# Kernel optimization log

Measured on AMD Instinct MI355X. Metric: run time of the kernel, lower is better.

The kernel has to match this reference:

```python
import jax, jax.numpy as jnp
import numpy as np

B, L, N, DM = 32, 12, 883, 64
DSP, DTP, H, HID, HOR = 128, 128, 4, 64, 12
E_SPA = 14128
ENC_LAYERS = 3
HIDDEN = 5 * HID  # 2*embed + node + tid + diw = 320


def _gat(x, es, et, W, a_s, a_d, bias, edge_att=None):
    # GATConv-style attention with optional per-edge info-bottleneck mask (gat_ib)
    n = x.shape[0]
    h = (x @ W).reshape(n, H, -1)            # [n,H,Dh]
    sc_s = (h * a_s).sum(-1)                 # [n,H]
    sc_d = (h * a_d).sum(-1)
    al = jax.nn.leaky_relu(sc_s[es] + sc_d[et], 0.2)   # [E,H]
    al = al - jax.ops.segment_max(al, et, num_segments=n)[et]
    ex = jnp.exp(al)
    a = ex / jax.ops.segment_sum(ex, et, num_segments=n)[et]
    if edge_att is not None:
        a = a * edge_att[:, None]
    out = jax.ops.segment_sum(a[..., None] * h[es], et, num_segments=n)
    return out.reshape(n, -1) + bias


def _gsat(x, ei, gat_p, ext_p):
    # GSAT: embed -> extractor MLP on edge endpoint pairs -> sigmoid edge att -> masked conv
    es, et = ei[0], ei[1]
    emb = _gat(x, es, et, *gat_p)
    w1, b1, w2, b2, w3, b3 = ext_p
    f = jnp.concatenate([emb[es], emb[et]], axis=-1)
    logit = (jax.nn.relu(jax.nn.relu(f @ w1 + b1) @ w2 + b2) @ w3 + b3)[:, 0]
    att = jax.nn.sigmoid(logit)  # eval-mode (no concrete-relaxation sampling)
    return _gat(x, es, et, *gat_p, edge_att=att)


def setup_inputs():
    key = jax.random.key(0)
    ks = iter(jax.random.split(key, 80))
    def nrm(shape, s=0.02):
        return jax.random.normal(next(ks), shape, jnp.float32) * s
    hist = jax.random.normal(next(ks), (B, L, N, 3), jnp.float32)
    tid = jax.random.randint(next(ks), (B, L, N), 0, 288).astype(jnp.float32)
    diw = jax.random.randint(next(ks), (B, L, N), 0, 7).astype(jnp.float32)
    hist = hist.at[..., 1].set(tid).at[..., 2].set(diw)
    ei_spa = jax.random.randint(next(ks), (2, E_SPA), 0, N).astype(jnp.int32)
    g = jnp.arange(L, dtype=jnp.int32)
    ei_temp = jnp.stack([jnp.repeat(g, L), jnp.tile(g, L)])  # dense lag x lag temporal graph
    inp = dict(history_data=hist, edge_idx_spa=ei_spa, edge_idx_temp=ei_temp)
    inp.update(
        node_emb=nrm((N, HID)), tid_emb=nrm((288, HID)), diw_emb=nrm((7, HID)),
        start_w=nrm((3, DM)), start_b=jnp.zeros((DM,), jnp.float32),
        ts_w=nrm((DM * L, HID)), ts_b=jnp.zeros((HID,), jnp.float32),
        tr_spat_w=nrm((L * DM, DSP)), tr_spat_b=jnp.zeros((DSP,), jnp.float32),
        inv_spat_w=nrm((DSP, L * DM)), inv_spat_b=jnp.zeros((L * DM,), jnp.float32),
        tr_temp_w=nrm((N * DM, DTP)), tr_temp_b=jnp.zeros((DTP,), jnp.float32),
        inv_temp_w=nrm((DTP, N * DM)), inv_temp_b=jnp.zeros((N * DM,), jnp.float32),
        gat_sp_w=nrm((DSP, DSP)), gat_sp_asrc=nrm((H, DSP // H)), gat_sp_adst=nrm((H, DSP // H)), gat_sp_bias=jnp.zeros((DSP,), jnp.float32),
        ext_sp_w1=nrm((2 * DSP, 4 * DSP)), ext_sp_b1=jnp.zeros((4 * DSP,), jnp.float32),
        ext_sp_w2=nrm((4 * DSP, DSP)), ext_sp_b2=jnp.zeros((DSP,), jnp.float32),
        ext_sp_w3=nrm((DSP, 1)), ext_sp_b3=jnp.zeros((1,), jnp.float32),
        gat_tp_w=nrm((DTP, DTP)), gat_tp_asrc=nrm((H, DTP // H)), gat_tp_adst=nrm((H, DTP // H)), gat_tp_bias=jnp.zeros((DTP,), jnp.float32),
        ext_tp_w1=nrm((2 * DTP, 4 * DTP)), ext_tp_b1=jnp.zeros((4 * DTP,), jnp.float32),
        ext_tp_w2=nrm((4 * DTP, DTP)), ext_tp_b2=jnp.zeros((DTP,), jnp.float32),
        ext_tp_w3=nrm((DTP, 1)), ext_tp_b3=jnp.zeros((1,), jnp.float32),
        enc_w1=nrm((ENC_LAYERS, HIDDEN, HIDDEN)), enc_b1=jnp.zeros((ENC_LAYERS, HIDDEN), jnp.float32),
        enc_w2=nrm((ENC_LAYERS, HIDDEN, HIDDEN)), enc_b2=jnp.zeros((ENC_LAYERS, HIDDEN), jnp.float32),
        reg_w=nrm((HIDDEN, HOR)), reg_b=jnp.zeros((HOR,), jnp.float32),
    )
    return inp


def reference(history_data, edge_idx_spa, edge_idx_temp, node_emb, tid_emb, diw_emb,
              start_w, start_b, ts_w, ts_b,
              tr_spat_w, tr_spat_b, inv_spat_w, inv_spat_b,
              tr_temp_w, tr_temp_b, inv_temp_w, inv_temp_b,
              gat_sp_w, gat_sp_asrc, gat_sp_adst, gat_sp_bias,
              ext_sp_w1, ext_sp_b1, ext_sp_w2, ext_sp_b2, ext_sp_w3, ext_sp_b3,
              gat_tp_w, gat_tp_asrc, gat_tp_adst, gat_tp_bias,
              ext_tp_w1, ext_tp_b1, ext_tp_w2, ext_tp_b2, ext_tp_w3, ext_tp_b3,
              enc_w1, enc_b1, enc_w2, enc_b2, reg_w, reg_b):
    b, l, n = history_data.shape[:3]
    tid = jax.lax.stop_gradient(history_data[:, -1, :, 1]).astype(jnp.int32)
    diw = jax.lax.stop_gradient(history_data[:, -1, :, 2]).astype(jnp.int32)
    X = history_data[..., :3] @ start_w + start_b           # [B,L,N,DM]
    res = X.transpose(0, 2, 1, 3).reshape(b, n, l * DM)      # [B,N,L*DM]
    ts_res = res @ ts_w + ts_b                               # conv1x1 over nodes == per-node linear
    gp_sp = (gat_sp_w, gat_sp_asrc, gat_sp_adst, gat_sp_bias)
    ep_sp = (ext_sp_w1, ext_sp_b1, ext_sp_w2, ext_sp_b2, ext_sp_w3, ext_sp_b3)
    gp_tp = (gat_tp_w, gat_tp_asrc, gat_tp_adst, gat_tp_bias)
    ep_tp = (ext_tp_w1, ext_tp_b1, ext_tp_w2, ext_tp_b2, ext_tp_w3, ext_tp_b3)
    # batch_st_gsat: per-sample spatial GSAT then temporal GSAT (vmapped instead of Python loop)
    spa_in = res @ tr_spat_w + tr_spat_b                     # [B,N,DSP]
    spa_out = jax.vmap(lambda xx: _gsat(xx, edge_idx_spa, gp_sp, ep_sp))(spa_in)
    spa_back = (spa_out @ inv_spat_w + inv_spat_b).reshape(b, n, l, DM).transpose(0, 2, 1, 3)
    temp_in = spa_back.reshape(b, l, n * DM) @ tr_temp_w + tr_temp_b   # [B,L,DTP]
    temp_out = jax.vmap(lambda xx: _gsat(xx, edge_idx_temp, gp_tp, ep_tp))(temp_in)
    temp_back = (temp_out @ inv_temp_w + inv_temp_b).reshape(b, l, n, DM)
    ts_temp = temp_back.transpose(0, 2, 1, 3).reshape(b, n, l * DM) @ ts_w + ts_b
    hid = jnp.concatenate([
        ts_res, ts_temp,
        jnp.broadcast_to(node_emb, (b, n, HID)),
        tid_emb[tid], diw_emb[diw],
    ], axis=-1)                                              # [B,N,320]
    for i in range(ENC_LAYERS):  # MLP_res: x + fc2(relu(fc1(x)))
        hid = hid + jax.nn.relu(hid @ enc_w1[i] + enc_b1[i]) @ enc_w2[i] + enc_b2[i]
    pred = hid @ reg_w + reg_b                               # [B,N,HOR]
    return pred.transpose(0, 2, 1)[..., None]                # [B,HOR,N,1]
```

## Files before the change

kernel.cpp:

```cpp
#include <hip/hip_runtime.h>
#include <hip/hip_bf16.h>
#include <cstdint>
#include <cstddef>

#define B_   32
#define L_   12
#define N_   883
#define DM_  64
#define E_SP 14128
#define E_TP 144
#define NT_  12
#define RBN  28256
#define RBL  384
#define LDM  768
#define NDM  56512

static inline int cdiv_h(int a, int b){ return (a+b-1)/b; }

__device__ __forceinline__ ushort f2bf(float f){
    unsigned u = __float_as_uint(f);
    unsigned lsb = (u >> 16) & 1u;
    u += 0x7fffu + lsb;
    return (ushort)(u >> 16);
}
__device__ __forceinline__ float bf2f(ushort h){
    return __uint_as_float(((unsigned)h) << 16);
}
__device__ __forceinline__ ushort f2h(float f){
    _Float16 h = (_Float16)f;
    ushort r; __builtin_memcpy(&r, &h, 2);
    return r;
}

typedef __bf16 bf16x8 __attribute__((ext_vector_type(8)));
typedef _Float16 f16x8 __attribute__((ext_vector_type(8)));
typedef _Float16 f16x2 __attribute__((ext_vector_type(2)));
typedef float  f32x4  __attribute__((ext_vector_type(4)));
typedef short  s16x2  __attribute__((ext_vector_type(2)));
union BF8 { bf16x8 v; ushort u[8]; unsigned w[4]; int4 i; };
union HF8 { f16x8 v; ushort u[8]; unsigned w[4]; int4 i; };

__device__ __forceinline__ unsigned pkrelu(unsigned x){
    s16x2 v;
    __builtin_memcpy(&v, &x, 4);
    s16x2 z = 0;
    v = __builtin_elementwise_max(v, z);
    unsigned r;
    __builtin_memcpy(&r, &v, 4);
    return r;
}
__device__ __forceinline__ unsigned pkaddh(unsigned x, unsigned y){
    f16x2 a, b;
    __builtin_memcpy(&a, &x, 4);
    __builtin_memcpy(&b, &y, 4);
    a = a + b;
    unsigned r;
    __builtin_memcpy(&r, &a, 4);
    return r;
}

__global__ void k_res(const float* __restrict__ hist, const float* __restrict__ sw,
                      const float* __restrict__ sb, ushort* __restrict__ resHi,
                      ushort* __restrict__ resLo)
{
    int idx = blockIdx.x*256 + threadIdx.x;
    if (idx >= RBN*LDM) return;
    int r = idx / LDM, col = idx - r*LDM;
    int b = r / N_, n = r - b*N_;
    int l = col >> 6, d = col & 63;
    const float* hp = hist + ((size_t)(b*L_ + l)*N_ + n)*3;
    float v = hp[0]*sw[d] + hp[1]*sw[64+d] + hp[2]*sw[128+d] + sb[d];
    ushort hi = f2bf(v);
    resHi[idx] = hi;
    resLo[idx] = f2bf(v - bf2f(hi));
}

template<int CT, int AMODE, int EPI, bool RELU, bool RES>
__launch_bounds__(256)
__global__ void mgemm(const ushort* __restrict__ A, const ushort* __restrict__ WT,
                      const float* __restrict__ bias, float* __restrict__ resF,
                      void* __restrict__ outP, int M, int N, int K)
{
    const int t = threadIdx.x, wv = t >> 6, l = t & 63;
    const int lr = l & 15, lk = l >> 4;
    const int row0 = blockIdx.y*64 + wv*16;
    const int col0 = blockIdx.x * (CT*16);
    int arr = row0 + lr; if (arr >= M) arr = M-1;
    int ab = 0, an = 0;
    if (AMODE == 1) { ab = arr / N_; an = arr - ab*N_; }
    const ushort* ap = A + (size_t)arr*K + lk*8;
    f32x4 acc[CT] = {};
    for (int k0 = 0; k0 < K; k0 += 32) {
        BF8 af;
        if (AMODE == 0) af.i = *(const int4*)(ap + k0);
        else {
            int k = k0 + lk*8; int ll = k >> 6, d = k & 63;
            af.i = *(const int4*)(A + ((size_t)(ab*L_ + ll))*NDM + (size_t)an*64 + d);
        }
        #pragma unroll
        for (int ct = 0; ct < CT; ++ct) {
            BF8 bf; bf.i = *(const int4*)&WT[(size_t)(col0 + ct*16 + lr)*K + k0 + lk*8];
            acc[ct] = __builtin_amdgcn_mfma_f32_16x16x32_bf16(af.v, bf.v, acc[ct], 0, 0, 0);
        }
    }
    #pragma unroll
    for (int ct = 0; ct < CT; ++ct) {
        int c = col0 + ct*16 + lr;
        float bv = 0.f;
        if (EPI == 2) { if (bias && c < 12) bv = bias[c]; }
        else if (bias) bv = bias[c];
        #pragma unroll
        for (int g = 0; g < 4; ++g) {
            int r = row0 + lk*4 + g;
            if (r >= M) continue;
            float v = acc[ct][g] + bv;
            if (RELU) v = fmaxf(v, 0.f);
            if (RES) {
                v += resF[(size_t)r*N + c];
                resF[(size_t)r*N + c] = v;
            }
            if (EPI == 0) {
                ((ushort*)outP)[(size_t)r*N + c] = f2bf(v);
            } else if (EPI == 1) {
                ((float*)outP)[(size_t)r*N + c] = v;
            } else if (EPI == 2) {
                if (c < 12) {
                    int b = r / N_, n = r - (r/N_)*N_;
                    ((float*)outP)[((size_t)(b*L_ + c))*N_ + n] = v;
                }
            } else {
                int b = r / N_, n = r - (r/N_)*N_;
                ((ushort*)outP)[((size_t)(b*L_ + (c>>6)))*NDM + (size_t)n*64 + (c&63)] = f2bf(v);
            }
        }
    }
}

template<int RT, int CT, int EPI, bool RELU, bool RES>
__launch_bounds__(256)
__global__ void mgemm_rt(const ushort* __restrict__ A, const ushort* __restrict__ WT,
                         const float* __restrict__ bias, float* __restrict__ resF,
                         void* __restrict__ outP, int M, int N, int K)
{
    const int t = threadIdx.x, wv = t >> 6, l = t & 63;
    const int lr = l & 15, lk = l >> 4;
    const int rowbase = blockIdx.y*(4*RT*16) + wv*(RT*16);
    const int col0 = blockIdx.x * (CT*16);
    const ushort* ap[RT];
    #pragma unroll
    for (int rt = 0; rt < RT; ++rt) {
        int arr = rowbase + rt*16 + lr; if (arr >= M) arr = M-1;
        ap[rt] = A + (size_t)arr*K + lk*8;
    }
    f32x4 acc[RT][CT] = {};
    for (int k0 = 0; k0 < K; k0 += 32) {
        BF8 af[RT];
        #pragma unroll
        for (int rt = 0; rt < RT; ++rt) af[rt].i = *(const int4*)(ap[rt] + k0);
        #pragma unroll
        for (int ct = 0; ct < CT; ++ct) {
            BF8 bf; bf.i = *(const int4*)&WT[(size_t)(col0 + ct*16 + lr)*K + k0 + lk*8];
            #pragma unroll
            for (int rt = 0; rt < RT; ++rt)
                acc[rt][ct] = __builtin_amdgcn_mfma_f32_16x16x32_bf16(af[rt].v, bf.v,
                                                                     acc[rt][ct], 0, 0, 0);
        }
    }
    #pragma unroll
    for (int rt = 0; rt < RT; ++rt)
        #pragma unroll
        for (int ct = 0; ct < CT; ++ct) {
            int c = col0 + ct*16 + lr;
            float bv = bias ? bias[c] : 0.f;
            #pragma unroll
            for (int g = 0; g < 4; ++g) {
                int r = rowbase + rt*16 + lk*4 + g;
                if (r >= M) continue;
                float v = acc[rt][ct][g] + bv;
                if (RELU) v = fmaxf(v, 0.f);
                if (RES) {
                    v += resF[(size_t)r*N + c];
                    resF[(size_t)r*N + c] = v;
                }
                if (EPI == 0) {
                    ((ushort*)outP)[(size_t)r*N + c] = f2bf(v);
                } else if (EPI == 1) {
                    ((float*)outP)[(size_t)r*N + c] = v;
                } else if (EPI == 4) {
                    ((ushort*)outP)[(size_t)r*N + c] = f2h(v);
                } else {
                    int b = r / N_, n = r - (r/N_)*N_;
                    ((ushort*)outP)[((size_t)(b*L_ + (c>>6)))*NDM + (size_t)n*64 + (c&63)] = f2bf(v);
                }
            }
        }
}

template<int CT>
__launch_bounds__(256)
__global__ void mgemm_hl(const ushort* __restrict__ Ahi, const ushort* __restrict__ Alo,
                         const ushort* __restrict__ WThi, const ushort* __restrict__ WTlo,
                         const float* __restrict__ bias, float* __restrict__ outF,
                         int M, int N, int K)
{
    const int t = threadIdx.x, wv = t >> 6, l = t & 63;
    const int lr = l & 15, lk = l >> 4;
    const int row0 = blockIdx.y*64 + wv*16;
    const int col0 = blockIdx.x * (CT*16);
    int arr = row0 + lr; if (arr >= M) arr = M-1;
    const ushort* aph = Ahi + (size_t)arr*K + lk*8;
    const ushort* apl = Alo + (size_t)arr*K + lk*8;
    f32x4 acc[CT] = {};
    for (int k0 = 0; k0 < K; k0 += 32) {
        BF8 ah, al_;
        ah.i  = *(const int4*)(aph + k0);
        al_.i = *(const int4*)(apl + k0);
        #pragma unroll
        for (int ct = 0; ct < CT; ++ct) {
            size_t wo = (size_t)(col0 + ct*16 + lr)*K + k0 + lk*8;
            BF8 bh, bl;
            bh.i = *(const int4*)&WThi[wo];
            bl.i = *(const int4*)&WTlo[wo];
            acc[ct] = __builtin_amdgcn_mfma_f32_16x16x32_bf16(ah.v,  bh.v, acc[ct], 0, 0, 0);
            acc[ct] = __builtin_amdgcn_mfma_f32_16x16x32_bf16(al_.v, bh.v, acc[ct], 0, 0, 0);
            acc[ct] = __builtin_amdgcn_mfma_f32_16x16x32_bf16(ah.v,  bl.v, acc[ct], 0, 0, 0);
        }
    }
    #pragma unroll
    for (int ct = 0; ct < CT; ++ct) {
        int c = col0 + ct*16 + lr;
        float bv = bias ? bias[c] : 0.f;
        #pragma unroll
        for (int g = 0; g < 4; ++g) {
            int r = row0 + lk*4 + g;
            if (r >= M) continue;
            outF[(size_t)r*N + c] = acc[ct][g] + bv;
        }
    }
}

#define TCH 1024
__launch_bounds__(256)
__global__ void temp_in_mfma(const ushort* __restrict__ AT, const ushort* __restrict__ WtT,
                             float* __restrict__ out)
{
    const int t = threadIdx.x, wv = t >> 6, l = t & 63;
    const int lr = l & 15, lk = l >> 4;
    const int row0 = blockIdx.y * 96;
    const int c0 = wv * 32;
    const int k0b = blockIdx.x * TCH;
    const int kend = (k0b + TCH < NDM) ? (k0b + TCH) : NDM;
    f32x4 acc[6][2] = {};
    for (int k0 = k0b; k0 < kend; k0 += 32) {
        BF8 b0, b1;
        b0.i = *(const int4*)&WtT[(size_t)(c0 + lr)*NDM + k0 + lk*8];
        b1.i = *(const int4*)&WtT[(size_t)(c0 + 16 + lr)*NDM + k0 + lk*8];
        #pragma unroll
        for (int m = 0; m < 6; ++m) {
            BF8 af; af.i = *(const int4*)&AT[(size_t)(row0 + m*16 + lr)*NDM + k0 + lk*8];
            acc[m][0] = __builtin_amdgcn_mfma_f32_16x16x32_bf16(af.v, b0.v, acc[m][0], 0, 0, 0);
            acc[m][1] = __builtin_amdgcn_mfma_f32_16x16x32_bf16(af.v, b1.v, acc[m][1], 0, 0, 0);
        }
    }
    #pragma unroll
    for (int m = 0; m < 6; ++m)
        #pragma unroll
        for (int ct = 0; ct < 2; ++ct) {
            int c = c0 + ct*16 + lr;
            #pragma unroll
            for (int g = 0; g < 4; ++g) {
                int r = row0 + m*16 + lk*4 + g;
                atomicAdd(&out[(size_t)r*128 + c], acc[m][ct][g]);
            }
        }
}

__global__ void k_sc(const ushort* __restrict__ h, const float* __restrict__ as_,
                     const float* __restrict__ ad_, float* __restrict__ scs,
                     float* __restrict__ scd, int R)
{
    int r = blockIdx.x*256 + threadIdx.x;
    if (r >= R) return;
    const ushort* hr = h + (size_t)r*128;
    #pragma unroll
    for (int hh = 0; hh < 4; ++hh) {
        float ss = 0.f, sd = 0.f;
        #pragma unroll
        for (int k = 0; k < 32; ++k) {
            float hv = bf2f(hr[hh*32 + k]);
            ss += hv*as_[hh*32+k];
            sd += hv*ad_[hh*32+k];
        }
        scs[(size_t)r*4+hh] = ss;
        scd[(size_t)r*4+hh] = sd;
    }
}

__global__ void k_attE(const float* __restrict__ scs, const float* __restrict__ scd,
                       const int* __restrict__ ei, int E, int NN,
                       float* __restrict__ a_buf, float* __restrict__ nsum)
{
    int idx = blockIdx.x*256 + threadIdx.x;
    if (idx >= B_*E) return;
    int b = idx / E, e = idx - b*E;
    int s = ei[e], tg = ei[E+e];
    const float* ps = scs + (size_t)(b*NN+s)*4;
    const float* pd = scd + (size_t)(b*NN+tg)*4;
    float* ns = nsum + (size_t)(b*NN+tg)*4;
    float* pa = a_buf + (size_t)idx*4;
    #pragma unroll
    for (int hh = 0; hh < 4; ++hh) {
        float al = ps[hh] + pd[hh];
        al = al > 0.f ? al : 0.2f*al;
        float ex = expf(al);
        pa[hh] = ex;
        atomicAdd(ns + hh, ex);
    }
}

__global__ void k_count(const int* __restrict__ ei, int E, int* __restrict__ counts){
    int e = blockIdx.x*256 + threadIdx.x;
    if (e < E) atomicAdd(&counts[ei[E + e]], 1);
}
__global__ void k_scan(const int* __restrict__ counts, int* __restrict__ off,
                       int* __restrict__ cur, int n)
{
    __shared__ int s[1024];
    int t = threadIdx.x;
    int v0 = (t < n) ? counts[t] : 0;
    s[t] = v0;
    __syncthreads();
    for (int o = 1; o < 1024; o <<= 1) {
        int v = (t >= o) ? s[t-o] : 0;
        __syncthreads();
        s[t] += v;
        __syncthreads();
    }
    if (t < n) {
        off[t+1] = s[t];
        cur[t] = s[t] - v0;
        if (t == 0) off[0] = 0;
    }
}
__global__ void k_fill(const int* __restrict__ ei, int E, int* __restrict__ cur,
                       int* __restrict__ lst){
    int e = blockIdx.x*256 + threadIdx.x;
    if (e < E) {
        int pos = atomicAdd(&cur[ei[E+e]], 1);
        lst[pos] = e;
    }
}

template<bool USE_ATT>
__global__ void k_gather(const ushort* __restrict__ h, const float* __restrict__ a_buf,
                         const float* __restrict__ nsum, const float* __restrict__ att,
                         const int* __restrict__ ei, const int* __restrict__ off,
                         const int* __restrict__ lst, const float* __restrict__ bias,
                         ushort* __restrict__ out, int E, int NN)
{
    int bn = blockIdx.x*4 + (threadIdx.x >> 6);
    int b = bn / NN, n = bn - b*NN;
    int lane = threadIdx.x & 63;
    int c0 = lane*2;
    int hh = lane >> 4;
    float rn = 1.f / nsum[(size_t)bn*4 + hh];
    int o0 = off[n], o1 = off[n+1];
    float ax = 0.f, ay = 0.f;
    for (int i = o0; i < o1; ++i) {
        int e = lst[i];
        float a = a_buf[((size_t)b*E + e)*4 + hh] * rn;
        if (USE_ATT) a *= att[(size_t)b*E + e];
        int s = ei[e];
        unsigned hv = *(const unsigned*)&h[((size_t)b*NN + s)*128 + c0];
        ax += a * __uint_as_float(hv << 16);
        ay += a * __uint_as_float(hv & 0xffff0000u);
    }
    ushort2 o2;
    o2.x = f2bf(ax + bias[c0]);
    o2.y = f2bf(ay + bias[c0+1]);
    *(ushort2*)&out[(size_t)bn*128 + c0] = o2;
}

__global__ void k_prepW2(const float* __restrict__ W2, ushort* __restrict__ W2T)
{
    int idx = blockIdx.x*256 + threadIdx.x;
    if (idx >= 512*128) return;
    int k = idx >> 7, c = idx & 127;
    W2T[(size_t)c*512 + k] = f2h(W2[idx]);
}
__global__ void k_prepT(const float* __restrict__ W, ushort* __restrict__ WT, int K, int N)
{
    int idx = blockIdx.x*256 + threadIdx.x;
    if (idx >= K*N) return;
    int k = idx / N, c = idx - k*N;
    WT[(size_t)c*K + k] = f2bf(W[idx]);
}
__global__ void k_prepT_hl(const float* __restrict__ W, ushort* __restrict__ WThi,
                           ushort* __restrict__ WTlo, int K, int N)
{
    int idx = blockIdx.x*256 + threadIdx.x;
    if (idx >= K*N) return;
    int k = idx / N, c = idx - k*N;
    float v = W[idx];
    ushort hi = f2bf(v);
    WThi[(size_t)c*K + k] = hi;
    WTlo[(size_t)c*K + k] = f2bf(v - bf2f(hi));
}
__global__ void k_prepWtT(const float* __restrict__ W, ushort* __restrict__ WT)
{
    __shared__ ushort tile[128][129];
    int k0 = blockIdx.x * 128;
    int t = threadIdx.x;
    for (int i = t; i < 128*128; i += 256) {
        int k = i >> 7, c = i & 127;
        int kk = k0 + k;
        tile[c][k] = (kk < NDM) ? f2bf(W[(size_t)kk*128 + c]) : (ushort)0;
    }
    __syncthreads();
    for (int i = t; i < 128*128; i += 256) {
        int c = i >> 7, k = i & 127;
        int kk = k0 + k;
        if (kk < NDM) WT[(size_t)c*NDM + kk] = tile[c][k];
    }
}
__global__ void k_prepT_big(const float* __restrict__ W, ushort* __restrict__ WT)
{
    __shared__ float tile[128][65];
    int c0 = blockIdx.x * 64;
    int t = threadIdx.x;
    for (int i = t; i < 128*64; i += 256) {
        int k = i >> 6, ci = i & 63;
        tile[k][ci] = W[(size_t)k*NDM + c0 + ci];
    }
    __syncthreads();
    for (int i = t; i < 64*128; i += 256) {
        int ci = i >> 7, k = i & 127;
        WT[(size_t)(c0 + ci)*128 + k] = f2bf(tile[k][ci]);
    }
}
__global__ void k_bcat(const float* __restrict__ b1, float* __restrict__ dst){
    int i = blockIdx.x*256 + threadIdx.x;
    if (i < 1024) dst[i] = (i < 512) ? b1[i] : 0.f;
}

template<bool SWZ>
__launch_bounds__(256, 3)
__global__ void ext2_mfma(const ushort* __restrict__ PQ, const ushort* __restrict__ W2T,
                          const float* __restrict__ b2, const float* __restrict__ w3,
                          const float* __restrict__ b3p, const int* __restrict__ ei,
                          const int* __restrict__ lst,
                          float* __restrict__ att, int E, int NN, int nblk)
{
    __shared__ ushort Bs[2][128*40];
    int bid = blockIdx.x;
    if (SWZ) {
        bid = (blockIdx.x & 7) * (gridDim.x >> 3) + (blockIdx.x >> 3);
        if (bid >= nblk) bid = nblk - 1;
    }
    const int t = threadIdx.x;
    const int wv = t >> 6, l = t & 63;
    const int lr = l & 15, lk = l >> 4;

    const ushort* pr[2]; const ushort* qr[2];
    int row0[2];
    #pragma unroll
    for (int rt = 0; rt < 2; ++rt) {
        row0[rt] = bid*128 + wv*32 + rt*16;
        int r = row0[rt] + lr;
        int b = (int)((unsigned)r / (unsigned)E), i = r - b*E;
        int e = lst[i];
        pr[rt] = PQ + ((size_t)b*NN + ei[e])*1024 + lk*8;
        qr[rt] = PQ + ((size_t)b*NN + ei[E+e])*1024 + 512 + lk*8;
    }
    const int sc = t >> 1, sh = (t & 1) * 16;
    const ushort* wsrc = W2T + (size_t)sc*512 + sh;
    ushort* wd0 = &Bs[0][sc*40 + sh];
    ushort* wd1 = &Bs[1][sc*40 + sh];

    {
        int4 a0 = *(const int4*)(wsrc);
        int4 a1 = *(const int4*)(wsrc + 8);
        *(int4*)wd0 = a0;
        *(int4*)(wd0 + 8) = a1;
    }
    HF8 pu[2], qu[2];
    #pragma unroll
    for (int rt = 0; rt < 2; ++rt) {
        pu[rt].i = *(const int4*)(pr[rt]);
        qu[rt].i = *(const int4*)(qr[rt]);
    }
    int4 bnA = *(const int4*)(wsrc + 32);
    int4 bnB = *(const int4*)(wsrc + 40);
    __syncthreads();

    f32x4 acc[2][8] = {};
    for (int kc = 0; kc < 16; ++kc) {
        const int cb = kc & 1;
        HF8 af[2];
        #pragma unroll
        for (int rt = 0; rt < 2; ++rt)
            #pragma unroll
            for (int j = 0; j < 4; ++j)
                af[rt].w[j] = pkrelu(pkaddh(pu[rt].w[j], qu[rt].w[j]));
        {
            int ka = (kc+1 < 15) ? kc+1 : 15;
            #pragma unroll
            for (int rt = 0; rt < 2; ++rt) {
                pu[rt].i = *(const int4*)(pr[rt] + ka*32);
                qu[rt].i = *(const int4*)(qr[rt] + ka*32);
            }
        }
        __builtin_amdgcn_s_setprio(1);
        #pragma unroll
        for (int ct = 0; ct < 8; ++ct) {
            HF8 bfm;
            bfm.v = *(const f16x8*)&Bs[cb][(ct*16 + lr)*40 + lk*8];
            #pragma unroll
            for (int rt = 0; rt < 2; ++rt)
                acc[rt][ct] = __builtin_amdgcn_mfma_f32_16x16x32_f16(af[rt].v, bfm.v,
                                                                    acc[rt][ct], 0, 0, 0);
        }
        __builtin_amdgcn_s_setprio(0);
        if (kc < 15) {
            ushort* wd = cb ? wd0 : wd1;
            *(int4*)wd = bnA;
            *(int4*)(wd + 8) = bnB;
        }
        {
            int kb = (kc+2 < 15) ? kc+2 : 15;
            bnA = *(const int4*)(wsrc + kb*32);
            bnB = *(const int4*)(wsrc + kb*32 + 8);
        }
        __syncthreads();
    }
    float b3 = b3p[0];
    #pragma unroll
    for (int rt = 0; rt < 2; ++rt) {
        float part[4] = {0.f,0.f,0.f,0.f};
        #pragma unroll
        for (int ct = 0; ct < 8; ++ct) {
            int c = ct*16 + lr;
            float b2v = b2[c], w3v = w3[c];
            #pragma unroll
            for (int g = 0; g < 4; ++g)
                part[g] += fmaxf(acc[rt][ct][g] + b2v, 0.f) * w3v;
        }
        #pragma unroll
        for (int m = 1; m < 16; m <<= 1)
            #pragma unroll
            for (int g = 0; g < 4; ++g)
                part[g] += __shfl_xor(part[g], m, 64);
        if (lr == 0) {
            #pragma unroll
            for (int g = 0; g < 4; ++g) {
                int rr = row0[rt] + lk*4 + g;
                int b = (int)((unsigned)rr / (unsigned)E), i = rr - b*E;
                int e = lst[i];
                att[(size_t)b*E + e] = 1.f/(1.f + expf(-(part[g] + b3)));
            }
        }
    }
}

__global__ void k_bias_fill(float* __restrict__ dst, const float* __restrict__ bias, int n){
    int i = blockIdx.x*256 + threadIdx.x;
    if (i < n) dst[i] = bias[i & 127];
}
__global__ void k_f2b(const float* __restrict__ src, ushort* __restrict__ dst, int n){
    int i = blockIdx.x*256 + threadIdx.x;
    if (i < n) dst[i] = f2bf(src[i]);
}

__global__ void k_hid(const float* __restrict__ ts_res, const float* __restrict__ ts_temp,
                      const float* __restrict__ node_emb, const float* __restrict__ tid_emb,
                      const float* __restrict__ diw_emb, const float* __restrict__ hist,
                      float* __restrict__ hid, ushort* __restrict__ hidB)
{
    int idx = blockIdx.x*256 + threadIdx.x;
    if (idx >= RBN*320) return;
    int r = idx / 320, c = idx - r*320;
    int b = r / N_, n = r - b*N_;
    float v;
    if (c < 64)        v = ts_res[(size_t)r*64 + c];
    else if (c < 128)  v = ts_temp[(size_t)r*64 + (c-64)];
    else if (c < 192)  v = node_emb[(size_t)n*64 + (c-128)];
    else if (c < 256) {
        int tid = (int)hist[((size_t)(b*L_ + (L_-1))*N_ + n)*3 + 1];
        v = tid_emb[(size_t)tid*64 + (c-192)];
    } else {
        int diw = (int)hist[((size_t)(b*L_ + (L_-1))*N_ + n)*3 + 2];
        v = diw_emb[(size_t)diw*64 + (c-256)];
    }
    hid[idx] = v;
    hidB[idx] = f2bf(v);
}

extern "C" void kernel_launch(void* const* d_in, const int* in_sizes, int n_in,
                              void* d_out, int out_size, void* d_ws, size_t ws_size,
                              hipStream_t stream)
{
    (void)in_sizes; (void)n_in; (void)out_size; (void)ws_size;
    const float* hist      = (const float*)d_in[0];
    const int*   ei_sp     = (const int*)  d_in[1];
    const int*   ei_tp     = (const int*)  d_in[2];
    const float* node_emb  = (const float*)d_in[3];
    const float* tid_emb   = (const float*)d_in[4];
    const float* diw_emb   = (const float*)d_in[5];
    const float* start_w   = (const float*)d_in[6];
    const float* start_b   = (const float*)d_in[7];
    const float* ts_w      = (const float*)d_in[8];
    const float* ts_b      = (const float*)d_in[9];
    const float* tr_spat_w = (const float*)d_in[10];
    const float* tr_spat_b = (const float*)d_in[11];
    const float* inv_spat_w= (const float*)d_in[12];
    const float* inv_spat_b= (const float*)d_in[13];
    const float* tr_temp_w = (const float*)d_in[14];
    const float* tr_temp_b = (const float*)d_in[15];
    const float* inv_temp_w= (const float*)d_in[16];
    const float* inv_temp_b= (const float*)d_in[17];
    const float* gat_sp_w  = (const float*)d_in[18];
    const float* gat_sp_as = (const float*)d_in[19];
    const float* gat_sp_ad = (const float*)d_in[20];
    const float* gat_sp_b  = (const float*)d_in[21];
    const float* ext_sp_w1 = (const float*)d_in[22];
    const float* ext_sp_b1 = (const float*)d_in[23];
    const float* ext_sp_w2 = (const float*)d_in[24];
    const float* ext_sp_b2 = (const float*)d_in[25];
    const float* ext_sp_w3 = (const float*)d_in[26];
    const float* ext_sp_b3 = (const float*)d_in[27];
    const float* gat_tp_w  = (const float*)d_in[28];
    const float* gat_tp_as = (const float*)d_in[29];
    const float* gat_tp_ad = (const float*)d_in[30];
    const float* gat_tp_b  = (const float*)d_in[31];
    const float* ext_tp_w1 = (const float*)d_in[32];
    const float* ext_tp_b1 = (const float*)d_in[33];
    const float* ext_tp_w2 = (const float*)d_in[34];
    const float* ext_tp_b2 = (const float*)d_in[35];
    const float* ext_tp_w3 = (const float*)d_in[36];
    const float* ext_tp_b3 = (const float*)d_in[37];
    const float* enc_w1    = (const float*)d_in[38];
    const float* enc_b1    = (const float*)d_in[39];
    const float* enc_w2    = (const float*)d_in[40];
    const float* enc_b2    = (const float*)d_in[41];
    const float* reg_w     = (const float*)d_in[42];
    const float* reg_b     = (const float*)d_in[43];
    float* out = (float*)d_out;

    size_t o = 0;
    char* wsb = (char*)d_ws;
    auto allocB = [&](size_t bytes) -> void* {
        void* p = wsb + o;
        o += (bytes + 255) & ~(size_t)255;
        return p;
    };
    void* bufA = allocB((size_t)RBN*768*2);
    void* bufB = allocB((size_t)RBN*768*2);
    void* bufC = allocB((size_t)RBN*512*2);
    void* bufD = allocB((size_t)RBN*320*2);
    float*  ts_res  = (float*)allocB((size_t)RBN*64*4);
    ushort* spaB    = (ushort*)allocB((size_t)RBN*128*2);
    ushort* hB      = (ushort*)allocB((size_t)RBN*128*2);
    float*  sc_s    = (float*)allocB((size_t)RBN*4*4);
    float*  sc_d    = (float*)allocB((size_t)RBN*4*4);
    float*  nsum    = (float*)allocB((size_t)RBN*4*4);
    float*  a_buf   = (float*)allocB((size_t)B_*E_SP*4*4);
    float*  att     = (float*)allocB((size_t)B_*E_SP*4);
    ushort* embB    = (ushort*)allocB((size_t)RBN*128*2);
    int*    csr     = (int*)allocB(17024*4);
    float*  temp_in = (float*)allocB((size_t)RBL*128*4);
    ushort* tempB   = (ushort*)allocB((size_t)RBL*128*2);
    ushort* toutB   = (ushort*)allocB((size_t)RBL*128*2);
    ushort* PQ_t    = (ushort*)allocB((size_t)RBL*1024*2);
    float*  ts_temp = (float*)allocB((size_t)RBN*64*4);
    ushort* W2T_sp  = (ushort*)allocB(512*128*2);
    ushort* W2T_tp  = (ushort*)allocB(512*128*2);
    ushort* WtT     = (ushort*)allocB((size_t)128*NDM*2);
    ushort* itWT    = (ushort*)allocB((size_t)NDM*128*2);
    ushort* tspWT   = (ushort*)allocB(128*768*2);
    ushort* ispWT   = (ushort*)allocB(768*128*2);
    ushort* gspWT   = (ushort*)allocB(128*128*2);
    ushort* gtpWT   = (ushort*)allocB(128*128*2);
    ushort* w1catT_sp = (ushort*)allocB((size_t)1024*128*2);
    ushort* w1catT_tp = (ushort*)allocB((size_t)1024*128*2);
    float*  b1cat_sp  = (float*)allocB(1024*4);
    float*  b1cat_tp  = (float*)allocB(1024*4);
    ushort* w1T_enc = (ushort*)allocB((size_t)3*320*320*2);
    ushort* w2T_enc = (ushort*)allocB((size_t)3*320*320*2);
    ushort* tswT_hi = (ushort*)allocB(64*768*2);
    ushort* tswT_lo = (ushort*)allocB(64*768*2);
    ushort* reg_wT  = (ushort*)allocB(16*320*2);

    ushort* resHi = (ushort*)bufA;
    ushort* resLo = (ushort*)bufB;
    ushort* AT    = (ushort*)bufA;
    float*  hid   = (float*)bufA;
    ushort* PQ_sp = (ushort*)bufB;
    ushort* tback = (ushort*)bufB;
    ushort* hidB  = (ushort*)bufC;
    ushort* R1b   = (ushort*)bufD;

    int* counts_sp = csr;
    int* off_sp    = csr + 883;
    int* cur_sp    = csr + 1767;
    int* list_sp   = csr + 2650;
    int* counts_tp = csr + 16778;
    int* off_tp    = csr + 16790;
    int* cur_tp    = csr + 16803;
    int* list_tp   = csr + 16815;

    hipMemsetAsync(counts_sp, 0, 883*4, stream);
    k_count<<<cdiv_h(E_SP,256),256,0,stream>>>(ei_sp, E_SP, counts_sp);
    k_scan<<<1,1024,0,stream>>>(counts_sp, off_sp, cur_sp, 883);
    k_fill<<<cdiv_h(E_SP,256),256,0,stream>>>(ei_sp, E_SP, cur_sp, list_sp);
    hipMemsetAsync(counts_tp, 0, 12*4, stream);
    k_count<<<1,256,0,stream>>>(ei_tp, E_TP, counts_tp);
    k_scan<<<1,1024,0,stream>>>(counts_tp, off_tp, cur_tp, 12);
    k_fill<<<1,256,0,stream>>>(ei_tp, E_TP, cur_tp, list_tp);
    k_prepW2<<<cdiv_h(512*128,256),256,0,stream>>>(ext_sp_w2, W2T_sp);
    k_prepW2<<<cdiv_h(512*128,256),256,0,stream>>>(ext_tp_w2, W2T_tp);
    k_prepWtT<<<cdiv_h(NDM,128),256,0,stream>>>(tr_temp_w, WtT);
    k_prepT_big<<<NDM/64,256,0,stream>>>(inv_temp_w, itWT);
    k_prepT<<<cdiv_h(768*128,256),256,0,stream>>>(tr_spat_w, tspWT, 768, 128);
    k_prepT<<<cdiv_h(128*768,256),256,0,stream>>>(inv_spat_w, ispWT, 128, 768);
    k_prepT<<<cdiv_h(128*128,256),256,0,stream>>>(gat_sp_w, gspWT, 128, 128);
    k_prepT<<<cdiv_h(128*128,256),256,0,stream>>>(gat_tp_w, gtpWT, 128, 128);
    k_prepT<<<cdiv_h(128*512,256),256,0,stream>>>(ext_sp_w1,           w1catT_sp,           128, 512);
    k_prepT<<<cdiv_h(128*512,256),256,0,stream>>>(ext_sp_w1 + 128*512, w1catT_sp + 512*128, 128, 512);
    k_prepT<<<cdiv_h(128*512,256),256,0,stream>>>(ext_tp_w1,           w1catT_tp,           128, 512);
    k_prepT<<<cdiv_h(128*512,256),256,0,stream>>>(ext_tp_w1 + 128*512, w1catT_tp + 512*128, 128, 512);
    k_bcat<<<4,256,0,stream>>>(ext_sp_b1, b1cat_sp);
    k_bcat<<<4,256,0,stream>>>(ext_tp_b1, b1cat_tp);
    for (int i = 0; i < 3; ++i) {
        k_prepT<<<cdiv_h(320*320,256),256,0,stream>>>(enc_w1 + (size_t)i*320*320, w1T_enc + (size_t)i*320*320, 320, 320);
        k_prepT<<<cdiv_h(320*320,256),256,0,stream>>>(enc_w2 + (size_t)i*320*320, w2T_enc + (size_t)i*320*320, 320, 320);
    }
    k_prepT_hl<<<cdiv_h(768*64,256),256,0,stream>>>(ts_w, tswT_hi, tswT_lo, 768, 64);
    hipMemsetAsync(reg_wT, 0, 16*320*2, stream);
    k_prepT<<<cdiv_h(320*12,256),256,0,stream>>>(reg_w, reg_wT, 320, 12);

    k_res<<<cdiv_h(RBN*LDM,256),256,0,stream>>>(hist, start_w, start_b, resHi, resLo);
    mgemm_hl<4><<<dim3(1,442),256,0,stream>>>(resHi, resLo, tswT_hi, tswT_lo, ts_b, ts_res,
                                              RBN, 64, LDM);
    mgemm_rt<2,4,0,false,false><<<dim3(2,221),256,0,stream>>>(resHi, tspWT, tr_spat_b, nullptr,
                                                              spaB, RBN, 128, LDM);

    mgemm_rt<2,4,0,false,false><<<dim3(2,221),256,0,stream>>>(spaB, gspWT, nullptr, nullptr,
                                                              hB, RBN, 128, 128);
    k_sc<<<cdiv_h(RBN,256),256,0,stream>>>(hB, gat_sp_as, gat_sp_ad, sc_s, sc_d, RBN);
    hipMemsetAsync(nsum, 0, (size_t)RBN*4*4, stream);
    k_attE<<<cdiv_h(B_*E_SP,256),256,0,stream>>>(sc_s, sc_d, ei_sp, E_SP, N_, a_buf, nsum);
    k_gather<false><<<RBN/4,256,0,stream>>>(hB, a_buf, nsum, nullptr, ei_sp, off_sp, list_sp,
                                            gat_sp_b, embB, E_SP, N_);
    mgemm_rt<2,8,4,false,false><<<dim3(8,221),256,0,stream>>>(embB, w1catT_sp, b1cat_sp, nullptr,
                                                              PQ_sp, RBN, 1024, 128);
    ext2_mfma<true><<<3536,256,0,stream>>>(PQ_sp, W2T_sp, ext_sp_b2, ext_sp_w3, ext_sp_b3,
                                           ei_sp, list_sp, att, E_SP, N_, (B_*E_SP)/128);
    k_gather<true><<<RBN/4,256,0,stream>>>(hB, a_buf, nsum, att, ei_sp, off_sp, list_sp,
                                           gat_sp_b, spaB, E_SP, N_);

    mgemm_rt<2,4,3,false,false><<<dim3(12,221),256,0,stream>>>(spaB, ispWT, inv_spat_b, nullptr,
                                                               AT, RBN, 768, 128);
    k_bias_fill<<<cdiv_h(RBL*128,256),256,0,stream>>>(temp_in, tr_temp_b, RBL*128);
    temp_in_mfma<<<dim3(56,4),256,0,stream>>>(AT, WtT, temp_in);
    k_f2b<<<cdiv_h(RBL*128,256),256,0,stream>>>(temp_in, tempB, RBL*128);

    mgemm_rt<2,4,0,false,false><<<dim3(2,3),256,0,stream>>>(tempB, gtpWT, nullptr, nullptr,
                                                            hB, RBL, 128, 128);
    k_sc<<<cdiv_h(RBL,256),256,0,stream>>>(hB, gat_tp_as, gat_tp_ad, sc_s, sc_d, RBL);
    hipMemsetAsync(nsum, 0, (size_t)RBL*4*4, stream);
    k_attE<<<cdiv_h(B_*E_TP,256),256,0,stream>>>(sc_s, sc_d, ei_tp, E_TP, NT_, a_buf, nsum);
    k_gather<false><<<RBL/4,256,0,stream>>>(hB, a_buf, nsum, nullptr, ei_tp, off_tp, list_tp,
                                            gat_tp_b, embB, E_TP, NT_);
    mgemm_rt<2,8,4,false,false><<<dim3(8,3),256,0,stream>>>(embB, w1catT_tp, b1cat_tp, nullptr,
                                                            PQ_t, RBL, 1024, 128);
    ext2_mfma<false><<<(B_*E_TP)/128,256,0,stream>>>(PQ_t, W2T_tp, ext_tp_b2, ext_tp_w3,
                                                     ext_tp_b3, ei_tp, list_tp, att, E_TP, NT_,
                                                     (B_*E_TP)/128);
    k_gather<true><<<RBL/4,256,0,stream>>>(hB, a_buf, nsum, att, ei_tp, off_tp, list_tp,
                                           gat_tp_b, toutB, E_TP, NT_);

    mgemm_rt<2,4,0,false,false><<<dim3(883,3),256,0,stream>>>(toutB, itWT, inv_temp_b, nullptr,
                                                              tback, RBL, NDM, 128);
    mgemm<4,1,1,false,false><<<dim3(1,442),256,0,stream>>>(tback, tswT_hi, ts_b, nullptr,
                                                           ts_temp, RBN, 64, LDM);

    k_hid<<<cdiv_h(RBN*320,256),256,0,stream>>>(ts_res, ts_temp, node_emb, tid_emb, diw_emb, hist,
                                                hid, hidB);
    for (int i = 0; i < 3; ++i) {
        mgemm_rt<2,5,0,true,false><<<dim3(4,221),256,0,stream>>>(hidB, w1T_enc + (size_t)i*320*320,
                                                                 enc_b1 + i*320, nullptr, R1b, RBN, 320, 320);
        mgemm_rt<2,5,0,false,true><<<dim3(4,221),256,0,stream>>>(R1b, w2T_enc + (size_t)i*320*320,
                                                                 enc_b2 + i*320, hid, hidB, RBN, 320, 320);
    }
    mgemm<1,0,2,false,false><<<dim3(1,442),256,0,stream>>>(hidB, reg_wT, reg_b, nullptr,
                                                           out, RBN, 16, 320);
}
```

Before: 1.407 ms.

## Fold start projection into ts/spatial weights and fuse GAT softmax into gather

Precomputes combined weights so the start linear layer (3->64 per lag) is folded algebraically into the ts_w and tr_spat_w projections. The front end then becomes a K=36 dot product per output, replacing the materialised 768-wide bf16 hi/lo residual and two GEMMs over it. The GAT edge-score kernel with its atomics and buffers is also removed, and exp and normalisation are recomputed inside the CSR gather. Costs are redundant exp work in the second gather, fp32 scalar front math instead of MFMA, and no max-subtraction in the softmax, which risks overflow.

Result: no change. 1.382 ms (-1.8%).

```diff
diff --git a/kernel.cpp b/kernel.cpp
--- a/kernel.cpp
+++ b/kernel.cpp
@@ -59,20 +59,62 @@
     return r;
 }
 
-__global__ void k_res(const float* __restrict__ hist, const float* __restrict__ sw,
-                      const float* __restrict__ sb, ushort* __restrict__ resHi,
-                      ushort* __restrict__ resLo)
+__global__ void k_mkA(const float* __restrict__ sw, const float* __restrict__ sb,
+                      const float* __restrict__ tsw, const float* __restrict__ tsb,
+                      const float* __restrict__ trsp, const float* __restrict__ trspb,
+                      float* __restrict__ A1, float* __restrict__ A2,
+                      float* __restrict__ cb1, float* __restrict__ cb2)
+{
+    int t = threadIdx.x;
+    for (int i = t; i < 36*64; i += 256) {
+        int k = i >> 6, h = i & 63;
+        int l = k/3, c = k - l*3;
+        float s = 0.f;
+        for (int d = 0; d < 64; ++d) s += sw[c*64+d]*tsw[(size_t)(l*64+d)*64 + h];
+        A1[i] = s;
+    }
+    for (int i = t; i < 36*128; i += 256) {
+        int k = i >> 7, p = i & 127;
+        int l = k/3, c = k - l*3;
+        float s = 0.f;
+        for (int d = 0; d < 64; ++d) s += sw[c*64+d]*trsp[(size_t)(l*64+d)*128 + p];
+        A2[i] = s;
+    }
+    for (int h = t; h < 64; h += 256) {
+        float s = tsb[h];
+        for (int k = 0; k < 768; ++k) s += sb[k & 63]*tsw[(size_t)k*64 + h];
+        cb1[h] = s;
+    }
+    for (int p = t; p < 128; p += 256) {
+        float s = trspb[p];
+        for (int k = 0; k < 768; ++k) s += sb[k & 63]*trsp[(size_t)k*128 + p];
+        cb2[p] = s;
+    }
+}
+__global__ void k_front(const float* __restrict__ hist, const float* __restrict__ A1,
+                        const float* __restrict__ A2, const float* __restrict__ cb1,
+                        const float* __restrict__ cb2, float* __restrict__ ts_res,
+                        ushort* __restrict__ spa_in)
 {
     int idx = blockIdx.x*256 + threadIdx.x;
-    if (idx >= RBN*LDM) return;
-    int r = idx / LDM, col = idx - r*LDM;
-    int b = r / N_, n = r - b*N_;
-    int l = col >> 6, d = col & 63;
-    const float* hp = hist + ((size_t)(b*L_ + l)*N_ + n)*3;
-    float v = hp[0]*sw[d] + hp[1]*sw[64+d] + hp[2]*sw[128+d] + sb[d];
-    ushort hi = f2bf(v);
-    resHi[idx] = hi;
-    resLo[idx] = f2bf(v - bf2f(hi));
+    if (idx >= RBN*192) return;
+    int bn = idx / 192, h = idx - bn*192;
+    int b = bn / N_, n = bn - b*N_;
+    const float* hp = hist + ((size_t)(b*L_)*N_ + n)*3;
+    bool isTs = (h < 64);
+    int hh = isTs ? h : (h - 64);
+    int stride = isTs ? 64 : 128;
+    const float* A = isTs ? (A1 + hh) : (A2 + hh);
+    float acc = isTs ? cb1[hh] : cb2[hh];
+    #pragma unroll
+    for (int l = 0; l < 12; ++l) {
+        float x0 = hp[l*2649 + 0];
+        float x1 = hp[l*2649 + 1];
+        float x2 = hp[l*2649 + 2];
+        acc += x0*A[(l*3+0)*stride] + x1*A[(l*3+1)*stride] + x2*A[(l*3+2)*stride];
+    }
+    if (isTs) ts_res[(size_t)bn*64 + hh] = acc;
+    else      spa_in[(size_t)bn*128 + hh] = f2bf(acc);
 }
 
 template<int CT, int AMODE, int EPI, bool RELU, bool RES>
@@ -196,49 +238,6 @@
         }
 }
 
-template<int CT>
-__launch_bounds__(256)
-__global__ void mgemm_hl(const ushort* __restrict__ Ahi, const ushort* __restrict__ Alo,
-                         const ushort* __restrict__ WThi, const ushort* __restrict__ WTlo,
-                         const float* __restrict__ bias, float* __restrict__ outF,
-                         int M, int N, int K)
-{
-    const int t = threadIdx.x, wv = t >> 6, l = t & 63;
-    const int lr = l & 15, lk = l >> 4;
-    const int row0 = blockIdx.y*64 + wv*16;
-    const int col0 = blockIdx.x * (CT*16);
-    int arr = row0 + lr; if (arr >= M) arr = M-1;
-    const ushort* aph = Ahi + (size_t)arr*K + lk*8;
-    const ushort* apl = Alo + (size_t)arr*K + lk*8;
-    f32x4 acc[CT] = {};
-    for (int k0 = 0; k0 < K; k0 += 32) {
-        BF8 ah, al_;
-        ah.i  = *(const int4*)(aph + k0);
-        al_.i = *(const int4*)(apl + k0);
-        #pragma unroll
-        for (int ct = 0; ct < CT; ++ct) {
-            size_t wo = (size_t)(col0 + ct*16 + lr)*K + k0 + lk*8;
-            BF8 bh, bl;
-            bh.i = *(const int4*)&WThi[wo];
-            bl.i = *(const int4*)&WTlo[wo];
-            acc[ct] = __builtin_amdgcn_mfma_f32_16x16x32_bf16(ah.v,  bh.v, acc[ct], 0, 0, 0);
-            acc[ct] = __builtin_amdgcn_mfma_f32_16x16x32_bf16(al_.v, bh.v, acc[ct], 0, 0, 0);
-            acc[ct] = __builtin_amdgcn_mfma_f32_16x16x32_bf16(ah.v,  bl.v, acc[ct], 0, 0, 0);
-        }
-    }
-    #pragma unroll
-    for (int ct = 0; ct < CT; ++ct) {
-        int c = col0 + ct*16 + lr;
-        float bv = bias ? bias[c] : 0.f;
-        #pragma unroll
-        for (int g = 0; g < 4; ++g) {
-            int r = row0 + lk*4 + g;
-            if (r >= M) continue;
-            outF[(size_t)r*N + c] = acc[ct][g] + bv;
-        }
-    }
-}
-
 #define TCH 1024
 __launch_bounds__(256)
 __global__ void temp_in_mfma(const ushort* __restrict__ AT, const ushort* __restrict__ WtT,
@@ -296,28 +295,6 @@
     }
 }
 
-__global__ void k_attE(const float* __restrict__ scs, const float* __restrict__ scd,
-                       const int* __restrict__ ei, int E, int NN,
-                       float* __restrict__ a_buf, float* __restrict__ nsum)
-{
-    int idx = blockIdx.x*256 + threadIdx.x;
-    if (idx >= B_*E) return;
-    int b = idx / E, e = idx - b*E;
-    int s = ei[e], tg = ei[E+e];
-    const float* ps = scs + (size_t)(b*NN+s)*4;
-    const float* pd = scd + (size_t)(b*NN+tg)*4;
-    float* ns = nsum + (size_t)(b*NN+tg)*4;
-    float* pa = a_buf + (size_t)idx*4;
-    #pragma unroll
-    for (int hh = 0; hh < 4; ++hh) {
-        float al = ps[hh] + pd[hh];
-        al = al > 0.f ? al : 0.2f*al;
-        float ex = expf(al);
-        pa[hh] = ex;
-        atomicAdd(ns + hh, ex);
-    }
-}
-
 __global__ void k_count(const int* __restrict__ ei, int E, int* __restrict__ counts){
     int e = blockIdx.x*256 + threadIdx.x;
     if (e < E) atomicAdd(&counts[ei[E + e]], 1);
@@ -352,8 +329,8 @@
 }
 
 template<bool USE_ATT>
-__global__ void k_gather(const ushort* __restrict__ h, const float* __restrict__ a_buf,
-                         const float* __restrict__ nsum, const float* __restrict__ att,
+__global__ void k_gather(const ushort* __restrict__ h, const float* __restrict__ scs,
+                         const float* __restrict__ scd, const float* __restrict__ att,
                          const int* __restrict__ ei, const int* __restrict__ off,
                          const int* __restrict__ lst, const float* __restrict__ bias,
                          ushort* __restrict__ out, int E, int NN)
@@ -363,21 +340,25 @@
     int lane = threadIdx.x & 63;
     int c0 = lane*2;
     int hh = lane >> 4;
-    float rn = 1.f / nsum[(size_t)bn*4 + hh];
+    float sd = scd[(size_t)bn*4 + hh];
     int o0 = off[n], o1 = off[n+1];
-    float ax = 0.f, ay = 0.f;
+    float ax = 0.f, ay = 0.f, sa = 0.f;
     for (int i = o0; i < o1; ++i) {
         int e = lst[i];
-        float a = a_buf[((size_t)b*E + e)*4 + hh] * rn;
-        if (USE_ATT) a *= att[(size_t)b*E + e];
         int s = ei[e];
+        float al = scs[(size_t)(b*NN + s)*4 + hh] + sd;
+        al = al > 0.f ? al : 0.2f*al;
+        float ex = expf(al);
+        sa += ex;
+        float a = USE_ATT ? ex * att[(size_t)b*E + e] : ex;
         unsigned hv = *(const unsigned*)&h[((size_t)b*NN + s)*128 + c0];
         ax += a * __uint_as_float(hv << 16);
         ay += a * __uint_as_float(hv & 0xffff0000u);
     }
+    float rn = (sa > 0.f) ? 1.f/sa : 0.f;
     ushort2 o2;
-    o2.x = f2bf(ax + bias[c0]);
-    o2.y = f2bf(ay + bias[c0+1]);
+    o2.x = f2bf(ax*rn + bias[c0]);
+    o2.y = f2bf(ay*rn + bias[c0+1]);
     *(ushort2*)&out[(size_t)bn*128 + c0] = o2;
 }
 
@@ -394,17 +375,6 @@
     if (idx >= K*N) return;
     int k = idx / N, c = idx - k*N;
     WT[(size_t)c*K + k] = f2bf(W[idx]);
-}
-__global__ void k_prepT_hl(const float* __restrict__ W, ushort* __restrict__ WThi,
-                           ushort* __restrict__ WTlo, int K, int N)
-{
-    int idx = blockIdx.x*256 + threadIdx.x;
-    if (idx >= K*N) return;
-    int k = idx / N, c = idx - k*N;
-    float v = W[idx];
-    ushort hi = f2bf(v);
-    WThi[(size_t)c*K + k] = hi;
-    WTlo[(size_t)c*K + k] = f2bf(v - bf2f(hi));
 }
 __global__ void k_prepWtT(const float* __restrict__ W, ushort* __restrict__ WT)
 {
@@ -662,8 +632,6 @@
     ushort* hB      = (ushort*)allocB((size_t)RBN*128*2);
     float*  sc_s    = (float*)allocB((size_t)RBN*4*4);
     float*  sc_d    = (float*)allocB((size_t)RBN*4*4);
-    float*  nsum    = (float*)allocB((size_t)RBN*4*4);
-    float*  a_buf   = (float*)allocB((size_t)B_*E_SP*4*4);
     float*  att     = (float*)allocB((size_t)B_*E_SP*4);
     ushort* embB    = (ushort*)allocB((size_t)RBN*128*2);
     int*    csr     = (int*)allocB(17024*4);
@@ -676,7 +644,6 @@
     ushort* W2T_tp  = (ushort*)allocB(512*128*2);
     ushort* WtT     = (ushort*)allocB((size_t)128*NDM*2);
     ushort* itWT    = (ushort*)allocB((size_t)NDM*128*2);
-    ushort* tspWT   = (ushort*)allocB(128*768*2);
     ushort* ispWT   = (ushort*)allocB(768*128*2);
     ushort* gspWT   = (ushort*)allocB(128*128*2);
     ushort* gtpWT   = (ushort*)allocB(128*128*2);
@@ -687,11 +654,12 @@
     ushort* w1T_enc = (ushort*)allocB((size_t)3*320*320*2);
     ushort* w2T_enc = (ushort*)allocB((size_t)3*320*320*2);
     ushort* tswT_hi = (ushort*)allocB(64*768*2);
-    ushort* tswT_lo = (ushort*)allocB(64*768*2);
     ushort* reg_wT  = (ushort*)allocB(16*320*2);
-
-    ushort* resHi = (ushort*)bufA;
-    ushort* resLo = (ushort*)bufB;
+    float*  A1      = (float*)allocB(36*64*4);
+    float*  A2      = (float*)allocB(36*128*4);
+    float*  cb1     = (float*)allocB(64*4);
+    float*  cb2     = (float*)allocB(128*4);
+
     ushort* AT    = (ushort*)bufA;
     float*  hid   = (float*)bufA;
     ushort* PQ_sp = (ushort*)bufB;
@@ -716,11 +684,12 @@
     k_count<<<1,256,0,stream>>>(ei_tp, E_TP, counts_tp);
     k_scan<<<1,1024,0,stream>>>(counts_tp, off_tp, cur_tp, 12);
     k_fill<<<1,256,0,stream>>>(ei_tp, E_TP, cur_tp, list_tp);
+    k_mkA<<<1,256,0,stream>>>(start_w, start_b, ts_w, ts_b, tr_spat_w, tr_spat_b,
+                              A1, A2, cb1, cb2);
     k_prepW2<<<cdiv_h(512*128,256),256,0,stream>>>(ext_sp_w2, W2T_sp);
     k_prepW2<<<cdiv_h(512*128,256),256,0,stream>>>(ext_tp_w2, W2T_tp);
     k_prepWtT<<<cdiv_h(NDM,128),256,0,stream>>>(tr_temp_w, WtT);
     k_prepT_big<<<NDM/64,256,0,stream>>>(inv_temp_w, itWT);
-    k_prepT<<<cdiv_h(768*128,256),256,0,stream>>>(tr_spat_w, tspWT, 768, 128);
     k_prepT<<<cdiv_h(128*768,256),256,0,stream>>>(inv_spat_w, ispWT, 128, 768);
     k_prepT<<<cdiv_h(128*128,256),256,0,stream>>>(gat_sp_w, gspWT, 128, 128);
     k_prepT<<<cdiv_h(128*128,256),256,0,stream>>>(gat_tp_w, gtpWT, 128, 128);
@@ -734,28 +703,22 @@
         k_prepT<<<cdiv_h(320*320,256),256,0,stream>>>(enc_w1 + (size_t)i*320*320, w1T_enc + (size_t)i*320*320, 320, 320);
         k_prepT<<<cdiv_h(320*320,256),256,0,stream>>>(enc_w2 + (size_t)i*320*320, w2T_enc + (size_t)i*320*320, 320, 320);
     }
-    k_prepT_hl<<<cdiv_h(768*64,256),256,0,stream>>>(ts_w, tswT_hi, tswT_lo, 768, 64);
+    k_prepT<<<cdiv_h(768*64,256),256,0,stream>>>(ts_w, tswT_hi, 768, 64);
     hipMemsetAsync(reg_wT, 0, 16*320*2, stream);
     k_prepT<<<cdiv_h(320*12,256),256,0,stream>>>(reg_w, reg_wT, 320, 12);
 
-    k_res<<<cdiv_h(RBN*LDM,256),256,0,stream>>>(hist, start_w, start_b, resHi, resLo);
-    mgemm_hl<4><<<dim3(1,442),256,0,stream>>>(resHi, resLo, tswT_hi, tswT_lo, ts_b, ts_res,
-                                              RBN, 64, LDM);
-    mgemm_rt<2,4,0,false,false><<<dim3(2,221),256,0,stream>>>(resHi, tspWT, tr_spat_b, nullptr,
-                                                              spaB, RBN, 128, LDM);
+    k_front<<<cdiv_h(RBN*192,256),256,0,stream>>>(hist, A1, A2, cb1, cb2, ts_res, spaB);
 
     mgemm_rt<2,4,0,false,false><<<dim3(2,221),256,0,stream>>>(spaB, gspWT, nullptr, nullptr,
                                                               hB, RBN, 128, 128);
     k_sc<<<cdiv_h(RBN,256),256,0,stream>>>(hB, gat_sp_as, gat_sp_ad, sc_s, sc_d, RBN);
-    hipMemsetAsync(nsum, 0, (size_t)RBN*4*4, stream);
-    k_attE<<<cdiv_h(B_*E_SP,256),256,0,stream>>>(sc_s, sc_d, ei_sp, E_SP, N_, a_buf, nsum);
-    k_gather<false><<<RBN/4,256,0,stream>>>(hB, a_buf, nsum, nullptr, ei_sp, off_sp, list_sp,
+    k_gather<false><<<RBN/4,256,0,stream>>>(hB, sc_s, sc_d, nullptr, ei_sp, off_sp, list_sp,
                                             gat_sp_b, embB, E_SP, N_);
     mgemm_rt<2,8,4,false,false><<<dim3(8,221),256,0,stream>>>(embB, w1catT_sp, b1cat_sp, nullptr,
                                                               PQ_sp, RBN, 1024, 128);
     ext2_mfma<true><<<3536,256,0,stream>>>(PQ_sp, W2T_sp, ext_sp_b2, ext_sp_w3, ext_sp_b3,
                                            ei_sp, list_sp, att, E_SP, N_, (B_*E_SP)/128);
-    k_gather<true><<<RBN/4,256,0,stream>>>(hB, a_buf, nsum, att, ei_sp, off_sp, list_sp,
+    k_gather<true><<<RBN/4,256,0,stream>>>(hB, sc_s, sc_d, att, ei_sp, off_sp, list_sp,
                                            gat_sp_b, spaB, E_SP, N_);
 
     mgemm_rt<2,4,3,false,false><<<dim3(12,221),256,0,stream>>>(spaB, ispWT, inv_spat_b, nullptr,
@@ -767,16 +730,14 @@
     mgemm_rt<2,4,0,false,false><<<dim3(2,3),256,0,stream>>>(tempB, gtpWT, nullptr, nullptr,
                                                             hB, RBL, 128, 128);
     k_sc<<<cdiv_h(RBL,256),256,0,stream>>>(hB, gat_tp_as, gat_tp_ad, sc_s, sc_d, RBL);
-    hipMemsetAsync(nsum, 0, (size_t)RBL*4*4, stream);
-    k_attE<<<cdiv_h(B_*E_TP,256),256,0,stream>>>(sc_s, sc_d, ei_tp, E_TP, NT_, a_buf, nsum);
-    k_gather<false><<<RBL/4,256,0,stream>>>(hB, a_buf, nsum, nullptr, ei_tp, off_tp, list_tp,
+    k_gather<false><<<RBL/4,256,0,stream>>>(hB, sc_s, sc_d, nullptr, ei_tp, off_tp, list_tp,
                                             gat_tp_b, embB, E_TP, NT_);
     mgemm_rt<2,8,4,false,false><<<dim3(8,3),256,0,stream>>>(embB, w1catT_tp, b1cat_tp, nullptr,
                                                             PQ_t, RBL, 1024, 128);
     ext2_mfma<false><<<(B_*E_TP)/128,256,0,stream>>>(PQ_t, W2T_tp, ext_tp_b2, ext_tp_w3,
                                                      ext_tp_b3, ei_tp, list_tp, att, E_TP, NT_,
                                                      (B_*E_TP)/128);
-    k_gather<true><<<RBL/4,256,0,stream>>>(hB, a_buf, nsum, att, ei_tp, off_tp, list_tp,
+    k_gather<true><<<RBL/4,256,0,stream>>>(hB, sc_s, sc_d, att, ei_tp, off_tp, list_tp,
                                            gat_tp_b, toutB, E_TP, NT_);
 
     mgemm_rt<2,4,0,false,false><<<dim3(883,3),256,0,stream>>>(toutB, itWT, inv_temp_b, nullptr,
```
